# Kernel tuning notes

Measured on AMD Instinct MI355X. Metric: run time of the kernel, lower is better.

The kernel has to match this reference:

```python
import jax, jax.numpy as jnp
import numpy as np

DILATION = 3
SUBSIZE = 16
TOPK = 16


def _forward(fm1, fm2):
    bs, c, h, w = fm1.shape
    d = min(h, w, DILATION)   # dilation clamp: sorted([h, w, dilation])[0]
    s = min(h, w, SUBSIZE)    # subsize clamp
    nby, nbx = h // s, w // s
    # non-overlapping sub-blocks of fm1: (bs, c, nby, nbx, s, s)
    blk = fm1.reshape(bs, c, nby, s, nbx, s).transpose(0, 1, 2, 4, 3, 5)
    ys = jnp.arange(nby) * s
    xs = jnp.arange(nbx) * s
    offs = jnp.arange(s)
    # all (dh, dw) shifts in [-d, d]^2
    dhs, dws = jnp.meshgrid(jnp.arange(-d, d + 1), jnp.arange(-d, d + 1), indexing='ij')
    shifts = jnp.stack([dhs.reshape(-1), dws.reshape(-1)], axis=-1)  # ((2d+1)^2, 2)
    denom = jnp.asarray(c * s * s, fm1.dtype)  # per-sample element count of a block

    def step(carry, shift):
        dh, dw = shift[0], shift[1]
        # boundary clamp of the fm2 window origin (matches the if/elif ladder)
        y0 = jnp.clip(ys + dh, 0, h - s)
        x0 = jnp.clip(xs + dw, 0, w - s)
        ri = y0[:, None] + offs[None, :]  # (nby, s)
        ci = x0[:, None] + offs[None, :]  # (nbx, s)
        # gathered fm2 windows: (bs, c, nby, nbx, s, s)
        win = fm2[:, :, ri[:, None, :, None], ci[None, :, None, :]]
        # per-sample MSE per block: sum over (c, s, s) / (c*s*s)
        dist = jnp.sum((blk - win) ** 2, axis=(1, 4, 5)) / denom  # (bs, nby, nbx)
        return jnp.minimum(carry, dist.reshape(bs, -1)), None

    init = jnp.full((bs, nby * nbx), jnp.inf, dtype=fm1.dtype)
    min_per_block, _ = jax.lax.scan(step, init, shifts)  # (bs, nblocks)

    nblocks = nby * nbx
    if 0 <= TOPK <= nblocks:
        # sum of the TOPK smallest block distances per sample
        smallest = -jax.lax.top_k(-min_per_block, TOPK)[0]
        return jnp.sum(smallest, axis=-1)
    return jnp.sum(min_per_block, axis=-1)


def setup_inputs() -> dict:
    key = jax.random.key(0)
    k1, k2 = jax.random.split(key)
    fm1 = jax.random.normal(k1, (8, 64, 192, 192), dtype=jnp.float32)
    fm2 = jax.random.normal(k2, (8, 64, 192, 192), dtype=jnp.float32)
    return {"fm1": fm1, "fm2": fm2}


def reference(fm1, fm2):
    return _forward(fm1, fm2)
```

## Files before the change

### kernel.cpp

```cpp
#include <hip/hip_runtime.h>
#include <math.h>

#define HH 192
#define WW 192
#define CC 64
#define CHW (HH*WW)
#define SS 16
#define NB 12
#define NBLK 144
#define CCH 8
#define UROW 22
#define LROW 28
#define QN 6
#define NSH 49
#define STAGE_N (CCH*UROW*QN)

__device__ __forceinline__ int iclamp(int v, int lo, int hi){ return v<lo?lo:(v>hi?hi:v); }

template<int EX, int OX, int NCH>
__device__ __forceinline__ void run_chunks(
    const float* __restrict__ f1b, const float* __restrict__ f2b,
    float* sm, int tid, int t, int y, int h8, bool active,
    int ys, int xs, int rbase, int ey, int cc0, float acc[7])
{
  const int cbase4 = (EX == -3) ? 0 : ((EX == 0) ? (xs - 4) : (WW - LROW + 4));
  const int oyt = iclamp(t + ey, 0, 6);
  const float* ap0 = f1b + (size_t)(ys + y)*WW + xs + h8;
  const int wrow = (y + oyt)*LROW + h8;

  for (int ch0 = 0; ch0 < NCH; ch0 += CCH) {
    const int cc = cc0 + ch0;
    for (int i = tid; i < STAGE_N; i += 256) {
      int ch  = i / (UROW*QN);
      int rem = i - ch*(UROW*QN);
      int r   = rem / QN;
      int q   = rem - r*QN;
      *(float4*)&sm[ch*(UROW*LROW) + r*LROW + 4*q] =
        *(const float4*)(f2b + (size_t)(cc+ch)*CHW + (size_t)(rbase+r)*WW + cbase4 + 4*q);
    }
    __syncthreads();

    if (active) {
#pragma unroll 2
      for (int c = 0; c < CCH; c++) {
        const float* ap = ap0 + (size_t)(cc + c)*CHW;
        float a[8];
        {
          float4 v0 = *(const float4*)(ap + 0);
          float4 v1 = *(const float4*)(ap + 4);
          a[0]=v0.x; a[1]=v0.y; a[2]=v0.z; a[3]=v0.w;
          a[4]=v1.x; a[5]=v1.y; a[6]=v1.z; a[7]=v1.w;
        }
        const float* wp = sm + c*(UROW*LROW) + wrow;
        float w[16];
#pragma unroll
        for (int j = 0; j < 4; j++) {
          float4 v = *(const float4*)(wp + 4*j);
          w[4*j]=v.x; w[4*j+1]=v.y; w[4*j+2]=v.z; w[4*j+3]=v.w;
        }
#pragma unroll
        for (int u = 0; u < 7; u++) {
          const int o = ((u+EX) < 0 ? 0 : ((u+EX) > 6 ? 6 : (u+EX))) + OX;
          float s0 = 0.f, s1 = 0.f;
#pragma unroll
          for (int x = 0; x < 8; x += 2) {
            float d0 = a[x]   - w[o+x];
            float d1 = a[x+1] - w[o+x+1];
            s0 = fmaf(d0, d0, s0);
            s1 = fmaf(d1, d1, s1);
          }
          acc[u] += s0 + s1;
        }
      }
    }
    __syncthreads();
  }
}

template<int NZ>
__global__ __launch_bounds__(256, 8) void dist_kernel(
    const float* __restrict__ fm1, const float* __restrict__ fm2,
    float* __restrict__ partial)
{
  __shared__ float sm[CCH*UROW*LROW];

  const int blk = blockIdx.x;
  const int b   = blockIdx.y;
  const int z   = blockIdx.z;
  const int by  = blk / NB, bx = blk - by*NB;
  const int ys  = by*SS, xs = bx*SS;
  const int rbase = iclamp(ys-3, 0, HH-UROW);
  const int ey = (ys-3) - rbase;

  const int tid = threadIdx.x;
  const int t   = tid >> 5;
  const int y   = (tid & 31) >> 1;
  const int h8  = (tid & 1) * 8;
  const bool active = (t < 7);

  const float* f1b = fm1 + (size_t)b*CC*CHW;
  const float* f2b = fm2 + (size_t)b*CC*CHW;

  const int cc0 = z * (CC/NZ);

  float acc[7];
#pragma unroll
  for (int k = 0; k < 7; k++) acc[k] = 0.f;

  if (bx == 0)
    run_chunks<-3,0,CC/NZ>(f1b, f2b, sm, tid, t, y, h8, active, ys, xs, rbase, ey, cc0, acc);
  else if (bx == NB-1)
    run_chunks< 3,2,CC/NZ>(f1b, f2b, sm, tid, t, y, h8, active, ys, xs, rbase, ey, cc0, acc);
  else
    run_chunks< 0,1,CC/NZ>(f1b, f2b, sm, tid, t, y, h8, active, ys, xs, rbase, ey, cc0, acc);

  float* distk = sm;
#pragma unroll
  for (int u = 0; u < 7; u++) {
    float v = acc[u];
#pragma unroll
    for (int off = 16; off; off >>= 1) v += __shfl_xor(v, off);
    if (active && (tid & 31) == 0) distk[t*7 + u] = v;
  }
  __syncthreads();

  if constexpr (NZ == 2) {
    if (tid < NSH)
      partial[((size_t)(b*NBLK + blk)*NZ + z)*NSH + tid] = distk[tid];
  } else {
    if (tid < 64) {
      float v = (tid < NSH) ? distk[tid] : __builtin_inff();
#pragma unroll
      for (int off = 32; off; off >>= 1) v = fminf(v, __shfl_xor(v, off));
      if (tid == 0) partial[(size_t)b*NBLK + blk] = v;
    }
  }
}

template<int NZ>
__global__ void topk_kernel(const float* __restrict__ partial, float* __restrict__ out)
{
  const int b = blockIdx.x;
  const int lane = threadIdx.x;
  const float INF = __builtin_inff();

  float v0 = INF, v1 = INF, v2 = INF;
  if constexpr (NZ == 2) {
#pragma unroll
    for (int i = 0; i < 3; i++) {
      int blk = lane + 64*i;
      if (blk < NBLK) {
        const float* p = partial + (size_t)(b*NBLK + blk)*2*NSH;
        float m = INF;
        for (int k = 0; k < NSH; k++) m = fminf(m, p[k] + p[k+NSH]);
        if (i == 0) v0 = m; else if (i == 1) v1 = m; else v2 = m;
      }
    }
  } else {
    const float* p = partial + (size_t)b*NBLK;
    v0 = p[lane];
    v1 = p[lane + 64];
    v2 = (lane < 16) ? p[lane + 128] : INF;
  }

  float sum = 0.f;
  for (int it = 0; it < 16; ++it) {
    float lm = fminf(v0, fminf(v1, v2));
    float m = lm;
#pragma unroll
    for (int off = 32; off; off >>= 1) m = fminf(m, __shfl_xor(m, off));
    sum += m;
    unsigned long long mask = __ballot(lm == m);
    int leader = __ffsll(mask) - 1;
    if (lane == leader) {
      if (v0 == m)      v0 = INF;
      else if (v1 == m) v1 = INF;
      else              v2 = INF;
    }
  }
  if (lane == 0) out[b] = sum * (1.0f/((float)CC*SS*SS));
}

extern "C" void kernel_launch(void* const* d_in, const int* in_sizes, int n_in,
                              void* d_out, int out_size, void* d_ws, size_t ws_size,
                              hipStream_t stream)
{
  const float* fm1 = (const float*)d_in[0];
  const float* fm2 = (const float*)d_in[1];
  float* out  = (float*)d_out;
  float* scratch = (float*)d_ws;

  const size_t NEED = (size_t)8 * NBLK * 2 * NSH * sizeof(float);
  if (ws_size >= NEED) {
    dist_kernel<2><<<dim3(NBLK, 8, 2), 256, 0, stream>>>(fm1, fm2, scratch);
    topk_kernel<2><<<8, 64, 0, stream>>>(scratch, out);
  } else {
    dist_kernel<1><<<dim3(NBLK, 8, 1), 256, 0, stream>>>(fm1, fm2, scratch);
    topk_kernel<1><<<8, 64, 0, stream>>>(scratch, out);
  }
}
```

Before: 118.4 us.

## Register-prefetch fm2 tiles and drop channel split across workgroups

```diff
diff --git a/kernel.cpp b/kernel.cpp
--- a/kernel.cpp
+++ b/kernel.cpp
@@ -14,52 +14,69 @@
 #define QN 6
 #define NSH 49
 #define STAGE_N (CCH*UROW*QN)
+#define PAD_IDX (CCH*UROW*LROW)
+#define LDS_FLOATS (PAD_IDX + 4)
 
 __device__ __forceinline__ int iclamp(int v, int lo, int hi){ return v<lo?lo:(v>hi?hi:v); }
 
-template<int EX, int OX, int NCH>
+template<int EX, int OX>
 __device__ __forceinline__ void run_chunks(
     const float* __restrict__ f1b, const float* __restrict__ f2b,
     float* sm, int tid, int t, int y, int h8, bool active,
-    int ys, int xs, int rbase, int ey, int cc0, float acc[7])
+    int ys, int xs, int rbase, int ey, float acc[7])
 {
   const int cbase4 = (EX == -3) ? 0 : ((EX == 0) ? (xs - 4) : (WW - LROW + 4));
+
+  int goff[5], lidx[5];
+#pragma unroll
+  for (int j = 0; j < 5; ++j) {
+    int i  = tid + 256*j;
+    bool v = (i < STAGE_N);
+    int iq = v ? i : 0;
+    int ch  = iq / (UROW*QN);
+    int rem = iq - ch*(UROW*QN);
+    int r   = rem / QN;
+    int q   = rem - r*QN;
+    goff[j] = ch*CHW + (rbase + r)*WW + cbase4 + 4*q;
+    lidx[j] = v ? (ch*(UROW*LROW) + r*LROW + 4*q) : PAD_IDX;
+  }
+
   const int oyt = iclamp(t + ey, 0, 6);
   const float* ap0 = f1b + (size_t)(ys + y)*WW + xs + h8;
   const int wrow = (y + oyt)*LROW + h8;
 
-  for (int ch0 = 0; ch0 < NCH; ch0 += CCH) {
-    const int cc = cc0 + ch0;
-    for (int i = tid; i < STAGE_N; i += 256) {
-      int ch  = i / (UROW*QN);
-      int rem = i - ch*(UROW*QN);
-      int r   = rem / QN;
-      int q   = rem - r*QN;
-      *(float4*)&sm[ch*(UROW*LROW) + r*LROW + 4*q] =
-        *(const float4*)(f2b + (size_t)(cc+ch)*CHW + (size_t)(rbase+r)*WW + cbase4 + 4*q);
+  float4 pf[5];
+#pragma unroll
+  for (int j = 0; j < 5; ++j) pf[j] = *(const float4*)(f2b + goff[j]);
+
+  for (int ck = 0; ck < CC/CCH; ++ck) {
+    __syncthreads();
+#pragma unroll
+    for (int j = 0; j < 5; ++j) *(float4*)&sm[lidx[j]] = pf[j];
+    if (ck + 1 < CC/CCH) {
+      const float* f2n = f2b + (size_t)(ck+1)*CCH*CHW;
+#pragma unroll
+      for (int j = 0; j < 5; ++j) pf[j] = *(const float4*)(f2n + goff[j]);
     }
     __syncthreads();
 
     if (active) {
+      const float* apc = ap0 + (size_t)ck*CCH*CHW;
 #pragma unroll 2
-      for (int c = 0; c < CCH; c++) {
-        const float* ap = ap0 + (size_t)(cc + c)*CHW;
-        float a[8];
-        {
-          float4 v0 = *(const float4*)(ap + 0);
-          float4 v1 = *(const float4*)(ap + 4);
-          a[0]=v0.x; a[1]=v0.y; a[2]=v0.z; a[3]=v0.w;
-          a[4]=v1.x; a[5]=v1.y; a[6]=v1.z; a[7]=v1.w;
-        }
+      for (int c = 0; c < CCH; ++c) {
+        const float* ap = apc + (size_t)c*CHW;
+        float4 v0 = *(const float4*)(ap + 0);
+        float4 v1 = *(const float4*)(ap + 4);
+        float a[8] = {v0.x,v0.y,v0.z,v0.w, v1.x,v1.y,v1.z,v1.w};
         const float* wp = sm + c*(UROW*LROW) + wrow;
         float w[16];
 #pragma unroll
-        for (int j = 0; j < 4; j++) {
-          float4 v = *(const float4*)(wp + 4*j);
-          w[4*j]=v.x; w[4*j+1]=v.y; w[4*j+2]=v.z; w[4*j+3]=v.w;
+        for (int jq = 0; jq < 4; ++jq) {
+          float4 vv = *(const float4*)(wp + 4*jq);
+          w[4*jq]=vv.x; w[4*jq+1]=vv.y; w[4*jq+2]=vv.z; w[4*jq+3]=vv.w;
         }
 #pragma unroll
-        for (int u = 0; u < 7; u++) {
+        for (int u = 0; u < 7; ++u) {
           const int o = ((u+EX) < 0 ? 0 : ((u+EX) > 6 ? 6 : (u+EX))) + OX;
           float s0 = 0.f, s1 = 0.f;
 #pragma unroll
@@ -73,20 +90,18 @@
         }
       }
     }
-    __syncthreads();
   }
 }
 
-template<int NZ>
-__global__ __launch_bounds__(256, 8) void dist_kernel(
+__global__ __launch_bounds__(256, 4) void dist_kernel(
     const float* __restrict__ fm1, const float* __restrict__ fm2,
     float* __restrict__ partial)
 {
-  __shared__ float sm[CCH*UROW*LROW];
+  __shared__ float sm[LDS_FLOATS];
 
-  const int blk = blockIdx.x;
-  const int b   = blockIdx.y;
-  const int z   = blockIdx.z;
+  const int wg  = blockIdx.x;
+  const int b   = wg & 7;
+  const int blk = wg >> 3;
   const int by  = blk / NB, bx = blk - by*NB;
   const int ys  = by*SS, xs = bx*SS;
   const int rbase = iclamp(ys-3, 0, HH-UROW);
@@ -101,22 +116,21 @@
   const float* f1b = fm1 + (size_t)b*CC*CHW;
   const float* f2b = fm2 + (size_t)b*CC*CHW;
 
-  const int cc0 = z * (CC/NZ);
-
   float acc[7];
 #pragma unroll
   for (int k = 0; k < 7; k++) acc[k] = 0.f;
 
   if (bx == 0)
-    run_chunks<-3,0,CC/NZ>(f1b, f2b, sm, tid, t, y, h8, active, ys, xs, rbase, ey, cc0, acc);
+    run_chunks<-3,0>(f1b, f2b, sm, tid, t, y, h8, active, ys, xs, rbase, ey, acc);
   else if (bx == NB-1)
-    run_chunks< 3,2,CC/NZ>(f1b, f2b, sm, tid, t, y, h8, active, ys, xs, rbase, ey, cc0, acc);
+    run_chunks< 3,2>(f1b, f2b, sm, tid, t, y, h8, active, ys, xs, rbase, ey, acc);
   else
-    run_chunks< 0,1,CC/NZ>(f1b, f2b, sm, tid, t, y, h8, active, ys, xs, rbase, ey, cc0, acc);
+    run_chunks< 0,1>(f1b, f2b, sm, tid, t, y, h8, active, ys, xs, rbase, ey, acc);
 
+  __syncthreads();
   float* distk = sm;
 #pragma unroll
-  for (int u = 0; u < 7; u++) {
+  for (int u = 0; u < 7; ++u) {
     float v = acc[u];
 #pragma unroll
     for (int off = 16; off; off >>= 1) v += __shfl_xor(v, off);
@@ -124,44 +138,24 @@
   }
   __syncthreads();
 
-  if constexpr (NZ == 2) {
-    if (tid < NSH)
-      partial[((size_t)(b*NBLK + blk)*NZ + z)*NSH + tid] = distk[tid];
-  } else {
-    if (tid < 64) {
-      float v = (tid < NSH) ? distk[tid] : __builtin_inff();
+  if (tid < 64) {
+    float v = (tid < NSH) ? distk[tid] : __builtin_inff();
 #pragma unroll
-      for (int off = 32; off; off >>= 1) v = fminf(v, __shfl_xor(v, off));
-      if (tid == 0) partial[(size_t)b*NBLK + blk] = v;
-    }
+    for (int off = 32; off; off >>= 1) v = fminf(v, __shfl_xor(v, off));
+    if (tid == 0) partial[(size_t)b*NBLK + blk] = v;
   }
 }
 
-template<int NZ>
 __global__ void topk_kernel(const float* __restrict__ partial, float* __restrict__ out)
 {
   const int b = blockIdx.x;
   const int lane = threadIdx.x;
   const float INF = __builtin_inff();
 
-  float v0 = INF, v1 = INF, v2 = INF;
-  if constexpr (NZ == 2) {
-#pragma unroll
-    for (int i = 0; i < 3; i++) {
-      int blk = lane + 64*i;
-      if (blk < NBLK) {
-        const float* p = partial + (size_t)(b*NBLK + blk)*2*NSH;
-        float m = INF;
-        for (int k = 0; k < NSH; k++) m = fminf(m, p[k] + p[k+NSH]);
-        if (i == 0) v0 = m; else if (i == 1) v1 = m; else v2 = m;
-      }
-    }
-  } else {
-    const float* p = partial + (size_t)b*NBLK;
-    v0 = p[lane];
-    v1 = p[lane + 64];
-    v2 = (lane < 16) ? p[lane + 128] : INF;
-  }
+  const float* p = partial + (size_t)b*NBLK;
+  float v0 = p[lane];
+  float v1 = p[lane + 64];
+  float v2 = (lane < 16) ? p[lane + 128] : INF;
 
   float sum = 0.f;
   for (int it = 0; it < 16; ++it) {
@@ -190,12 +184,6 @@
   float* out  = (float*)d_out;
   float* scratch = (float*)d_ws;
 
-  const size_t NEED = (size_t)8 * NBLK * 2 * NSH * sizeof(float);
-  if (ws_size >= NEED) {
-    dist_kernel<2><<<dim3(NBLK, 8, 2), 256, 0, stream>>>(fm1, fm2, scratch);
-    topk_kernel<2><<<8, 64, 0, stream>>>(scratch, out);
-  } else {
-    dist_kernel<1><<<dim3(NBLK, 8, 1), 256, 0, stream>>>(fm1, fm2, scratch);
-    topk_kernel<1><<<8, 64, 0, stream>>>(scratch, out);
-  }
+  dist_kernel<<<8*NBLK, 256, 0, stream>>>(fm1, fm2, scratch);
+  topk_kernel<<<8, 64, 0, stream>>>(scratch, out);
 }
```

New measurement: 128.9 us. 8.9% more time.
